# Performance work log

Measured on AMD Instinct MI355X. Metric: run time of the kernel, lower is better.

## Reference

```python
import jax, jax.numpy as jnp
import numpy as np

N = 32768          # total nodes
E = 262144         # edges (before self-loops)
F_IN = 128
H1, H2 = 512, 1024
G = 1024           # graphs (32 nodes each)
NUM_CLASSES = 20
EPS_BN = 1e-5
EPS_LN = 1e-5


def gcn_conv(x, src, dst, W, b, n):
    # PyG GCNConv: add self-loops, symmetric deg^-1/2 normalization,
    # aggregate at target (dst), bias added after aggregation.
    loops = jnp.arange(n)
    s = jnp.concatenate([src, loops])
    d = jnp.concatenate([dst, loops])
    xw = x @ W                                   # [n, out]
    deg = jax.ops.segment_sum(jnp.ones_like(d, dtype=xw.dtype), d, num_segments=n)
    dis = jnp.where(deg > 0, deg ** -0.5, 0.0)
    norm = dis[s] * dis[d]                       # [E+n]
    out = jax.ops.segment_sum(xw[s] * norm[:, None], d, num_segments=n)
    return out + b


def batch_norm(x, w, b):
    # training-mode BatchNorm1d over the node dimension (biased variance)
    mu = x.mean(axis=0)
    var = x.var(axis=0)
    return (x - mu) * jax.lax.rsqrt(var + EPS_BN) * w + b


def graph_layer_norm(x, w, b):
    # PyG LayerNorm(mode='graph') with batch=None: scalar mean/std over ALL
    # elements, eps added to std (not var), per-channel affine.
    mu = x.mean()
    std = jnp.sqrt(((x - mu) ** 2).mean())
    return (x - mu) / (std + EPS_LN) * w + b


def setup_inputs() -> dict:
    key = jax.random.key(0)
    ks = jax.random.split(key, 12)
    x = jax.random.normal(ks[0], (N, F_IN), dtype=jnp.float32)
    edge_index = jax.random.randint(ks[1], (2, E), 0, N, dtype=jnp.int64)
    batch = (jnp.arange(N, dtype=jnp.int64) // (N // G))  # 32 nodes per graph

    def glorot(k, shape):
        lim = np.sqrt(6.0 / (shape[0] + shape[1]))
        return jax.random.uniform(k, shape, jnp.float32, -lim, lim)

    return {
        "x": x,
        "edge_index": edge_index,
        "batch": batch,
        "conv1_w": glorot(ks[2], (F_IN, H1)),
        "conv1_b": jnp.zeros((H1,), jnp.float32),
        "bn1_w": jnp.ones((H1,), jnp.float32),
        "bn1_b": jnp.zeros((H1,), jnp.float32),
        "conv2_w": glorot(ks[3], (H1, H2)),
        "conv2_b": jnp.zeros((H2,), jnp.float32),
        "bn2_w": jnp.ones((H2,), jnp.float32),
        "bn2_b": jnp.zeros((H2,), jnp.float32),
        "ln1_w": jnp.ones((H2,), jnp.float32),
        "ln1_b": jnp.zeros((H2,), jnp.float32),
        "lin1_w": glorot(ks[4], (H2, H1)),
        "lin1_b": jnp.zeros((H1,), jnp.float32),
        "ln2_w": jnp.ones((H1,), jnp.float32),
        "ln2_b": jnp.zeros((H1,), jnp.float32),
        "lin2_w": glorot(ks[5], (H1, NUM_CLASSES)),
        "lin2_b": jnp.zeros((NUM_CLASSES,), jnp.float32),
    }


def reference(x, edge_index, batch, conv1_w, conv1_b, bn1_w, bn1_b,
              conv2_w, conv2_b, bn2_w, bn2_b, ln1_w, ln1_b,
              lin1_w, lin1_b, ln2_w, ln2_b, lin2_w, lin2_b):
    src, dst = edge_index[0], edge_index[1]
    h = jax.nn.relu(batch_norm(gcn_conv(x, src, dst, conv1_w, conv1_b, N), bn1_w, bn1_b))
    # dropout: eval mode -> identity
    h = jax.nn.relu(batch_norm(gcn_conv(h, src, dst, conv2_w, conv2_b, N), bn2_w, bn2_b))
    h = graph_layer_norm(h, ln1_w, ln1_b)
    pooled = jax.ops.segment_max(h, batch, num_segments=G)   # [G, H2]
    z = jax.nn.relu(pooled @ lin1_w + lin1_b)
    z = graph_layer_norm(z, ln2_w, ln2_b)
    logits = z @ lin2_w + lin2_b
    return jax.nn.log_softmax(logits, axis=1)
```

## Files before the change

kernel.cpp:

```cpp
#include <hip/hip_runtime.h>
#include <hip/hip_bf16.h>
#include <hip/hip_fp16.h>

#define NNODES 32768
#define NEDGES 262144
#define FIN    128
#define HID1   512
#define HID2   1024
#define NGRAPH 1024
#define NCLS   20
#define BCAP   64

typedef __attribute__((ext_vector_type(8))) short bf16x8;
typedef __attribute__((ext_vector_type(4))) float f32x4;
typedef __attribute__((ext_vector_type(2))) float f32x2;

__device__ inline float bf2f(unsigned short u) {
    union { unsigned int i; float f; } v; v.i = ((unsigned int)u) << 16; return v.f;
}
__device__ inline unsigned short f2bf(float f) {
    union { unsigned int i; float f; } v; v.f = f;
    unsigned int r = v.i + 0x7FFF + ((v.i >> 16) & 1);
    return (unsigned short)(r >> 16);
}

__device__ inline unsigned char f2e5(float f) {
    unsigned short h = __half_as_ushort(__float2half(f));
    unsigned short r = h + 0x7F + ((h >> 8) & 1);
    return (unsigned char)(r >> 8);
}
__device__ inline float e52f(unsigned char b) {
    return __half2float(__ushort_as_half((unsigned short)(b << 8)));
}

__device__ inline unsigned char f2e4(float f) {
    union { float f; unsigned int i; } v; v.f = f * 0x1p-120f;
    unsigned int b = v.i;
    unsigned int r = b + 0x7FFFF + ((b >> 20) & 1);
    return (unsigned char)(((r >> 20) & 0x7F) | ((b >> 24) & 0x80));
}
__device__ inline float e42f(unsigned char u) {
    union { unsigned int i; float f; } v;
    v.i = ((u & 0x80u) << 24) | ((u & 0x7Fu) << 20);
    return v.f * 0x1p+120f;
}

__device__ inline void e4x8_to_f32(uint2 u, float* v) {
#if __has_builtin(__builtin_amdgcn_cvt_pk_f32_fp8)
    f32x2 p0 = __builtin_amdgcn_cvt_pk_f32_fp8((int)u.x, false);
    f32x2 p1 = __builtin_amdgcn_cvt_pk_f32_fp8((int)u.x, true);
    f32x2 p2 = __builtin_amdgcn_cvt_pk_f32_fp8((int)u.y, false);
    f32x2 p3 = __builtin_amdgcn_cvt_pk_f32_fp8((int)u.y, true);
    v[0] = p0.x; v[1] = p0.y; v[2] = p1.x; v[3] = p1.y;
    v[4] = p2.x; v[5] = p2.y; v[6] = p3.x; v[7] = p3.y;
#else
    const unsigned char* up = (const unsigned char*)&u;
#pragma unroll
    for (int q = 0; q < 8; ++q) v[q] = e42f(up[q]);
#endif
}

typedef unsigned int u32g __attribute__((address_space(1)));
typedef unsigned int u32l __attribute__((address_space(3)));
__device__ inline void load16_lds(const void* g, void* l) {
    __builtin_amdgcn_global_load_lds((const u32g*)g, (u32l*)l, 16, 0, 0);
}

__device__ inline void wtrans_body(const float* __restrict__ W, unsigned short* __restrict__ Wt,
                                   int K, int N, int bx, int by, unsigned short (*tile)[72]) {
    int kb = by * 64, nb = bx * 64;
    {
        int k = threadIdx.x >> 2;
        int n0 = (threadIdx.x & 3) * 16;
#pragma unroll
        for (int q = 0; q < 4; ++q) {
            float4 v = *(const float4*)(W + (size_t)(kb + k) * N + nb + n0 + q * 4);
            tile[k][n0 + q * 4 + 0] = f2bf(v.x);
            tile[k][n0 + q * 4 + 1] = f2bf(v.y);
            tile[k][n0 + q * 4 + 2] = f2bf(v.z);
            tile[k][n0 + q * 4 + 3] = f2bf(v.w);
        }
    }
    __syncthreads();
    {
        int n = threadIdx.x >> 2;
        int k0 = (threadIdx.x & 3) * 16;
#pragma unroll
        for (int q = 0; q < 4; ++q) {
            ushort4 u;
            u.x = tile[k0 + q * 4 + 0][n];
            u.y = tile[k0 + q * 4 + 1][n];
            u.z = tile[k0 + q * 4 + 2][n];
            u.w = tile[k0 + q * 4 + 3][n];
            *(ushort4*)(Wt + (size_t)(nb + n) * K + kb + k0 + q * 4) = u;
        }
    }
}

__global__ __launch_bounds__(256) void prep(const float* __restrict__ x, unsigned short* __restrict__ xb,
                                            const float* __restrict__ W1, unsigned short* __restrict__ w1t,
                                            const float* __restrict__ W2, unsigned short* __restrict__ w2t,
                                            const float* __restrict__ W3, unsigned short* __restrict__ w3t,
                                            float* __restrict__ sF, int* __restrict__ cnt) {
    __shared__ unsigned short tile[64][72];
    int b = blockIdx.x;
    if (b < 168) {
        int t = b * 256 + threadIdx.x;
        if (t < 10240) sF[t] = 0.f;
        if (t < NNODES) cnt[t] = 0;
    } else if (b < 2216) {
        int i = (b - 168) * 256 + threadIdx.x;
        float4 a = ((const float4*)x)[i * 2];
        float4 c = ((const float4*)x)[i * 2 + 1];
        ushort4 u0, u1;
        u0.x = f2bf(a.x); u0.y = f2bf(a.y); u0.z = f2bf(a.z); u0.w = f2bf(a.w);
        u1.x = f2bf(c.x); u1.y = f2bf(c.y); u1.z = f2bf(c.z); u1.w = f2bf(c.w);
        ((ushort4*)xb)[i * 2] = u0;
        ((ushort4*)xb)[i * 2 + 1] = u1;
    } else if (b < 2232) {
        int q = b - 2216;
        wtrans_body(W1, w1t, FIN, HID1, q & 7, q >> 3, tile);
    } else if (b < 2360) {
        int q = b - 2232;
        wtrans_body(W2, w2t, HID1, HID2, q & 15, q >> 4, tile);
    } else {
        int q = b - 2360;
        wtrans_body(W3, w3t, HID2, HID1, q & 7, q >> 3, tile);
    }
}

__global__ __launch_bounds__(256) void bucket_fill(const int* __restrict__ src,
                                                   const int* __restrict__ dst,
                                                   int* __restrict__ cnt,
                                                   int* __restrict__ bucket) {
    int e = blockIdx.x * 256 + threadIdx.x;
    if (e >= NEDGES) return;
    int s = src[e], d = dst[e];
    int pos = atomicAdd(&cnt[d], 1);
    if (pos < BCAP) bucket[((size_t)d << 6) + pos] = s;
}

template<int F, int BNF, int XF8>
__global__ __launch_bounds__(256) void gcn_gather(const void* __restrict__ Xv,
                                                  const int* __restrict__ cnt,
                                                  const int* __restrict__ bucket,
                                                  const float* __restrict__ gsum,
                                                  const float* __restrict__ gsq,
                                                  const float* __restrict__ bw,
                                                  const float* __restrict__ bb,
                                                  float invN,
                                                  unsigned short* __restrict__ out) {
    constexpr int CPL = F / 64;
    int wave = threadIdx.x >> 6, lane = threadIdx.x & 63;
    int node = blockIdx.x * 4 + wave;
    int c0 = lane * CPL;
    float acc[CPL];
#pragma unroll
    for (int q = 0; q < CPL; ++q) acc[q] = 0.f;
    float sc[CPL], sh[CPL];
    if (BNF) {
#pragma unroll
        for (int q = 0; q < CPL; ++q) {
            int ch = c0 + q;
            float mu = gsum[ch] * invN;
            float var = gsq[ch] * invN - mu * mu;
            float s = rsqrtf(var + 1e-5f) * bw[ch];
            sc[q] = s;
            sh[q] = bb[ch] - mu * s;
        }
    }

    const unsigned short* Xc16 = (const unsigned short*)Xv + c0;
    const unsigned char*  Xc8  = (const unsigned char*)Xv + c0;

    auto accum = [&](int s, float w) {
        if (XF8) {
            uint2 u = *(const uint2*)(Xc8 + (size_t)s * F);
            float vv[8];
            e4x8_to_f32(u, vv);
#pragma unroll
            for (int q = 0; q < 8; ++q) {
                float v = vv[q];
                if (BNF) v = fmaxf(v * sc[q] + sh[q], 0.f);
                acc[q] += w * v;
            }
        } else if (CPL == 8) {
            int4 u = *(const int4*)(Xc16 + (size_t)s * F);
            const unsigned short* up = (const unsigned short*)&u;
#pragma unroll
            for (int q = 0; q < 8; ++q) {
                float v = bf2f(up[q]);
                if (BNF) v = fmaxf(v * sc[q] + sh[q], 0.f);
                acc[q] += w * v;
            }
        } else {
            ushort2 u = *(const ushort2*)(Xc16 + (size_t)s * F);
            float v0 = bf2f(u.x), v1 = bf2f(u.y);
            if (BNF) {
                v0 = fmaxf(v0 * sc[0] + sh[0], 0.f);
                v1 = fmaxf(v1 * sc[1] + sh[1], 0.f);
            }
            acc[0] += w * v0; acc[1] += w * v1;
        }
    };

    int deg = cnt[node];
    float di = rsqrtf((float)(deg + 1));
    accum(node, 1.0f / (float)(deg + 1));

    const int* bk = bucket + ((size_t)node << 6);
    int e = 0;
    for (; e + 8 <= deg; e += 8) {
        int4 s0 = *(const int4*)(bk + e);
        int4 s1 = *(const int4*)(bk + e + 4);
        int ss[8] = { s0.x, s0.y, s0.z, s0.w, s1.x, s1.y, s1.z, s1.w };
        float wv[8];
#pragma unroll
        for (int j = 0; j < 8; ++j) wv[j] = di * rsqrtf((float)(cnt[ss[j]] + 1));
#pragma unroll
        for (int j = 0; j < 8; ++j) accum(ss[j], wv[j]);
    }
    for (; e + 4 <= deg; e += 4) {
        int4 s0 = *(const int4*)(bk + e);
        int ss[4] = { s0.x, s0.y, s0.z, s0.w };
        float wv[4];
#pragma unroll
        for (int j = 0; j < 4; ++j) wv[j] = di * rsqrtf((float)(cnt[ss[j]] + 1));
#pragma unroll
        for (int j = 0; j < 4; ++j) accum(ss[j], wv[j]);
    }
    for (; e < deg; ++e) {
        int s = bk[e];
        accum(s, di * rsqrtf((float)(cnt[s] + 1)));
    }

    unsigned short* o = out + (size_t)node * F + c0;
    if (CPL == 2) {
        ushort2 u; u.x = f2bf(acc[0]); u.y = f2bf(acc[1]);
        *(ushort2*)o = u;
    } else {
        ushort4 u0, u1;
        u0.x = f2bf(acc[0]); u0.y = f2bf(acc[1]); u0.z = f2bf(acc[2]); u0.w = f2bf(acc[3]);
        u1.x = f2bf(acc[4]); u1.y = f2bf(acc[5]); u1.z = f2bf(acc[6]); u1.w = f2bf(acc[7]);
        *(ushort4*)o = u0;
        *(ushort4*)(o + 4) = u1;
    }
}

template<int BM, int EPI, int CBF16, int STATS, int POOL, int GSTATS, int CF8>
__global__ __launch_bounds__((BM == 128 ? 256 : 512), 2) void gemm_mfma(
        const unsigned short* __restrict__ A,
        const unsigned short* __restrict__ Bt,
        const float* __restrict__ bias,
        void* __restrict__ Cv,
        float* __restrict__ gsum,
        float* __restrict__ gsq,
        float* __restrict__ gmax,
        float* __restrict__ gmin,
        double* __restrict__ gacc,
        int M, int N, int K) {
    constexpr int BN = 128, BK = 64;
    constexpr int T = (BM == 128) ? 256 : 512;
    constexpr int SMEM_SH = (BM == 128) ? (128 * 136) : ((BM + BN) * BK);
    constexpr int AR = (BM * BK * 2) / (T * 16);
    constexpr int BR = (BN * BK * 2) / (T * 16);
    constexpr int RPR = T / 8;
    __shared__ unsigned short smem[SMEM_SH];
    unsigned short* As = smem;
    unsigned short* Bs = smem + BM * BK;

    const int tid = threadIdx.x;
    const int lane = tid & 63;
    const int wave = tid >> 6;
    const int wr = wave >> 1, wc = wave & 1;

    const int nwg = gridDim.x * gridDim.y;
    const int wg = blockIdx.y * gridDim.x + blockIdx.x;
    const int cpx = nwg >> 3;
    const int swz = (wg & 7) * cpx + (wg >> 3);
    const int m0 = (swz / gridDim.x) * BM, n0 = (swz % gridDim.x) * BN;

    const int sub = ((tid & 7) * 16) ^ (((tid >> 3) & 7) << 4);
    const int rbase = tid >> 3;
    const char* Ab = (const char*)A + sub;
    const char* Bb = (const char*)Bt + sub;

    f32x4 acc[4][4] = {};

    for (int k0 = 0; k0 < K; k0 += BK) {
        __syncthreads();
#pragma unroll
        for (int i = 0; i < AR; ++i) {
            int r = i * RPR + rbase;
            load16_lds(Ab + ((size_t)(m0 + r) * K + k0) * 2, (char*)As + i * (T * 16) + tid * 16);
        }
#pragma unroll
        for (int i = 0; i < BR; ++i) {
            int r = i * RPR + rbase;
            load16_lds(Bb + ((size_t)(n0 + r) * K + k0) * 2, (char*)Bs + i * (T * 16) + tid * 16);
        }
        __syncthreads();
#pragma unroll
        for (int ks = 0; ks < 2; ++ks) {
            bf16x8 af[4], bfr[4];
#pragma unroll
            for (int m = 0; m < 4; ++m) {
                int row = wr * 64 + m * 16 + (lane & 15);
                int s = (ks * 64 + ((lane >> 4) * 16)) ^ ((row & 7) << 4);
                af[m] = *(const bf16x8*)((const char*)As + row * 128 + s);
            }
#pragma unroll
            for (int n = 0; n < 4; ++n) {
                int row = wc * 64 + n * 16 + (lane & 15);
                int s = (ks * 64 + ((lane >> 4) * 16)) ^ ((row & 7) << 4);
                bfr[n] = *(const bf16x8*)((const char*)Bs + row * 128 + s);
            }
#pragma unroll
            for (int m = 0; m < 4; ++m)
#pragma unroll
                for (int n = 0; n < 4; ++n)
                    acc[m][n] = __builtin_amdgcn_mfma_f32_16x16x32_bf16(af[m], bfr[n], acc[m][n], 0, 0, 0);
        }
    }

    if (CBF16) {
        __syncthreads();
        unsigned char* ctile = (unsigned char*)smem;
        float cs[4], cq[4];
        float pmx[2][4], pmn[2][4];
#pragma unroll
        for (int n = 0; n < 4; ++n) {
            cs[n] = 0.f; cq[n] = 0.f;
            if (POOL) {
                pmx[0][n] = -1e30f; pmx[1][n] = -1e30f;
                pmn[0][n] = 1e30f;  pmn[1][n] = 1e30f;
            }
        }
#pragma unroll
        for (int n = 0; n < 4; ++n) {
            int col = wc * 64 + n * 16 + (lane & 15);
            float bsv = bias[n0 + col];
#pragma unroll
            for (int m = 0; m < 4; ++m) {
                int rbase2 = wr * 64 + m * 16 + ((lane >> 4) << 2);
#pragma unroll
                for (int j = 0; j < 4; ++j) {
                    float v = acc[m][n][j] + bsv;
                    if (STATS) { cs[n] += v; cq[n] += v * v; }
                    if (POOL) {
                        pmx[m >> 1][n] = fmaxf(pmx[m >> 1][n], v);
                        pmn[m >> 1][n] = fminf(pmn[m >> 1][n], v);
                    }
                    if (EPI == 1) v = fmaxf(v, 0.f);
                    if (CF8 == 1)      ctile[(rbase2 + j) * 144 + col] = f2e5(v);
                    else if (CF8 == 2) ctile[(rbase2 + j) * 144 + col] = f2e4(v);
                    else if (BM == 128) smem[(rbase2 + j) * 136 + col] = f2bf(v);
                }
            }
        }
        if (STATS) {
#pragma unroll
            for (int n = 0; n < 4; ++n) {
                cs[n] += __shfl_xor(cs[n], 16); cs[n] += __shfl_xor(cs[n], 32);
                cq[n] += __shfl_xor(cq[n], 16); cq[n] += __shfl_xor(cq[n], 32);
            }
            if (lane < 16) {
#pragma unroll
                for (int n = 0; n < 4; ++n) {
                    int col = n0 + wc * 64 + n * 16 + lane;
                    atomicAdd(&gsum[col], cs[n]);
                    atomicAdd(&gsq[col],  cq[n]);
                }
            }
        }
        if (POOL) {
#pragma unroll
            for (int gi = 0; gi < 2; ++gi)
#pragma unroll
                for (int n = 0; n < 4; ++n) {
                    pmx[gi][n] = fmaxf(pmx[gi][n], __shfl_xor(pmx[gi][n], 16));
                    pmx[gi][n] = fmaxf(pmx[gi][n], __shfl_xor(pmx[gi][n], 32));
                    pmn[gi][n] = fminf(pmn[gi][n], __shfl_xor(pmn[gi][n], 16));
                    pmn[gi][n] = fminf(pmn[gi][n], __shfl_xor(pmn[gi][n], 32));
                }
            if (lane < 16) {
                int gb = (m0 >> 5) + wr * 2;
#pragma unroll
                for (int gi = 0; gi < 2; ++gi)
#pragma unroll
                    for (int n = 0; n < 4; ++n) {
                        int col = n0 + wc * 64 + n * 16 + lane;
                        gmax[(size_t)(gb + gi) * HID2 + col] = pmx[gi][n];
                        gmin[(size_t)(gb + gi) * HID2 + col] = pmn[gi][n];
                    }
            }
        }
        __syncthreads();
        if (CF8) {
#pragma unroll
            for (int it = 0; it < (BM * 8) / T; ++it) {
                int l = it * T + tid;
                int r = l >> 3, ch = l & 7;
                int4 v = *(const int4*)(ctile + r * 144 + ch * 16);
                *(int4*)((unsigned char*)Cv + (size_t)(m0 + r) * N + n0 + ch * 16) = v;
            }
        } else if (BM == 128) {
#pragma unroll
            for (int it = 0; it < 8; ++it) {
                int r = it * 16 + (tid >> 4);
                int ch = tid & 15;
                int4 v = *(const int4*)&smem[r * 136 + ch * 8];
                *(int4*)((unsigned short*)Cv + (size_t)(m0 + r) * N + n0 + ch * 8) = v;
            }
        }
    } else {
        float ls = 0.f, lq = 0.f;
#pragma unroll
        for (int m = 0; m < 4; ++m) {
            int row = m0 + wr * 64 + m * 16 + ((lane >> 4) << 2);
#pragma unroll
            for (int n = 0; n < 4; ++n) {
                int col = n0 + wc * 64 + n * 16 + (lane & 15);
                float bsv = bias[col];
#pragma unroll
                for (int j = 0; j < 4; ++j) {
                    float v = acc[m][n][j] + bsv;
                    if (EPI == 1) v = fmaxf(v, 0.f);
                    if (GSTATS) { ls += v; lq += v * v; }
                    ((float*)Cv)[(size_t)(row + j) * N + col] = v;
                }
            }
        }
        if (GSTATS) {
            for (int o = 32; o > 0; o >>= 1) {
                ls += __shfl_down(ls, o);
                lq += __shfl_down(lq, o);
            }
            if (lane == 0) {
                atomicAdd(gacc,     (double)ls);
                atomicAdd(gacc + 1, (double)lq);
            }
        }
    }
}

__global__ __launch_bounds__(256) void lnstats_h2(const unsigned char* __restrict__ H,
                                                  const float* __restrict__ gsum,
                                                  const float* __restrict__ gsq,
                                                  const float* __restrict__ bw,
                                                  const float* __restrict__ bb,
                                                  float invN,
                                                  double* __restrict__ lnacc) {
    int half = threadIdx.x >> 7;
    int c0 = (threadIdx.x & 127) * 8;
    float sc[8], sh[8];
#pragma unroll
    for (int q = 0; q < 8; ++q) {
        int ch = c0 + q;
        float mu = gsum[ch] * invN;
        float var = gsq[ch] * invN - mu * mu;
        float s = rsqrtf(var + 1e-5f) * bw[ch];
        sc[q] = s;
        sh[q] = bb[ch] - mu * s;
    }
    float lsum = 0.f, lsq = 0.f;
    for (int r = blockIdx.x * 2 + half; r < NNODES; r += gridDim.x * 2) {
        uint2 u = *(const uint2*)(H + (size_t)r * HID2 + c0);
        const unsigned char* up = (const unsigned char*)&u;
#pragma unroll
        for (int q = 0; q < 8; ++q) {
            float v = fmaxf(e52f(up[q]) * sc[q] + sh[q], 0.f);
            lsum += v; lsq += v * v;
        }
    }
    for (int o = 32; o > 0; o >>= 1) {
        lsum += __shfl_down(lsum, o);
        lsq  += __shfl_down(lsq, o);
    }
    __shared__ float w1[4], w2[4];
    int wid = threadIdx.x >> 6, lane = threadIdx.x & 63;
    if (lane == 0) { w1[wid] = lsum; w2[wid] = lsq; }
    __syncthreads();
    if (threadIdx.x == 0) {
        atomicAdd(lnacc,     (double)(w1[0] + w1[1] + w1[2] + w1[3]));
        atomicAdd(lnacc + 1, (double)(w2[0] + w2[1] + w2[2] + w2[3]));
    }
}

__global__ __launch_bounds__(256) void pool_fin(const float* __restrict__ gmax,
                                                const float* __restrict__ gmin,
                                                const float* __restrict__ bsum,
                                                const float* __restrict__ bsq,
                                                const float* __restrict__ bw,
                                                const float* __restrict__ bb,
                                                const double* __restrict__ lnacc,
                                                const float* __restrict__ lw,
                                                const float* __restrict__ lb,
                                                float invN, double invCnt,
                                                unsigned short* __restrict__ P) {
    int i = blockIdx.x * 256 + threadIdx.x;
    int c0 = (i * 4) & (HID2 - 1);
    double dmu = lnacc[0] * invCnt;
    double dvar = lnacc[1] * invCnt - dmu * dmu;
    if (dvar < 0.0) dvar = 0.0;
    float smu = (float)dmu;
    float sinv = 1.0f / (sqrtf((float)dvar) + 1e-5f);
    float4 mx = ((const float4*)gmax)[i];
    float4 mn = ((const float4*)gmin)[i];
    float r[4];
    const float* mxp = (const float*)&mx;
    const float* mnp = (const float*)&mn;
#pragma unroll
    for (int q = 0; q < 4; ++q) {
        int ch = c0 + q;
        float bmu = bsum[ch] * invN;
        float bvar = bsq[ch] * invN - bmu * bmu;
        float s = rsqrtf(bvar + 1e-5f) * bw[ch];
        float t = bb[ch] - bmu * s;
        float A = sinv * lw[ch];
        float C = lb[ch] - smu * A;
        float vs = ((s >= 0.f) == (A >= 0.f)) ? mxp[q] : mnp[q];
        r[q] = A * fmaxf(s * vs + t, 0.f) + C;
    }
    ushort4 o;
    o.x = f2bf(r[0]); o.y = f2bf(r[1]); o.z = f2bf(r[2]); o.w = f2bf(r[3]);
    ((ushort4*)P)[i] = o;
}

__global__ __launch_bounds__(256) void gemm4_lsm(const float* __restrict__ Z,
                                                 const double* __restrict__ acc2,
                                                 const float* __restrict__ lw,
                                                 const float* __restrict__ lb,
                                                 const float* __restrict__ W,
                                                 const float* __restrict__ bias,
                                                 double invCnt,
                                                 float* __restrict__ out) {
    __shared__ float zs[HID1];
    __shared__ float part[8][NCLS];
    __shared__ float logits[NCLS];
    __shared__ float smaxs, slse;
    int m = blockIdx.x;
    double dmu = acc2[0] * invCnt;
    double dvar = acc2[1] * invCnt - dmu * dmu;
    if (dvar < 0.0) dvar = 0.0;
    float smu = (float)dmu;
    float sinv = 1.0f / (sqrtf((float)dvar) + 1e-5f);
    for (int k = threadIdx.x; k < HID1; k += 256) {
        float A = sinv * lw[k];
        zs[k] = Z[(size_t)m * HID1 + k] * A + (lb[k] - smu * A);
    }
    __syncthreads();
    int t = threadIdx.x;
    if (t < 160) {
        int c = t >> 3, s = t & 7;
        float a = 0.f;
        int k0 = s * 64;
#pragma unroll 8
        for (int k = k0; k < k0 + 64; ++k)
            a += zs[k] * W[k * NCLS + c];
        part[s][c] = a;
    }
    __syncthreads();
    if (t < NCLS) {
        float a = bias[t];
#pragma unroll
        for (int s = 0; s < 8; ++s) a += part[s][t];
        logits[t] = a;
    }
    __syncthreads();
    if (t == 0) {
        float mx = -1e30f;
        for (int j = 0; j < NCLS; ++j) mx = fmaxf(mx, logits[j]);
        float s = 0.f;
        for (int j = 0; j < NCLS; ++j) s += expf(logits[j] - mx);
        smaxs = mx; slse = logf(s);
    }
    __syncthreads();
    if (t < NCLS)
        out[(size_t)m * NCLS + t] = logits[t] - smaxs - slse;
}

extern "C" void kernel_launch(void* const* d_in, const int* in_sizes, int n_in,
                              void* d_out, int out_size, void* d_ws, size_t ws_size,
                              hipStream_t stream) {
    const float* x       = (const float*)d_in[0];
    const int*   ei      = (const int*)d_in[1];
    const int*   src     = ei;
    const int*   dst     = ei + NEDGES;
    const float* conv1_w = (const float*)d_in[3];
    const float* conv1_b = (const float*)d_in[4];
    const float* bn1_w   = (const float*)d_in[5];
    const float* bn1_b   = (const float*)d_in[6];
    const float* conv2_w = (const float*)d_in[7];
    const float* conv2_b = (const float*)d_in[8];
    const float* bn2_w   = (const float*)d_in[9];
    const float* bn2_b   = (const float*)d_in[10];
    const float* ln1_w   = (const float*)d_in[11];
    const float* ln1_b   = (const float*)d_in[12];
    const float* lin1_w  = (const float*)d_in[13];
    const float* lin1_b  = (const float*)d_in[14];
    const float* ln2_w   = (const float*)d_in[15];
    const float* ln2_b   = (const float*)d_in[16];
    const float* lin2_w  = (const float*)d_in[17];
    const float* lin2_b  = (const float*)d_in[18];
    float* out = (float*)d_out;

    char* ws = (char*)d_ws;
    const size_t KB = 1024, MB = 1048576;
    float*          sF      = (float*)(ws + 128 * KB);
    unsigned short* w1t     = (unsigned short*)(ws + 256 * KB);
    unsigned short* w2t     = (unsigned short*)(ws + 512 * KB);
    unsigned short* w3t     = (unsigned short*)(ws + 1536 * KB);
    int*            cnt     = (int*)(ws + 2560 * KB);
    unsigned short* pool    = (unsigned short*)(ws + 5 * MB);
    float*          z       = (float*)(ws + 7 * MB);
    unsigned short* agg1    = (unsigned short*)(ws + 16 * MB);
    unsigned char*  h1      = (unsigned char*)(ws + 24 * MB);
    unsigned char*  h2      = (unsigned char*)(ws + 16 * MB);
    int*            bucket  = (int*)(ws + 48 * MB);
    float*          gmax    = (float*)(ws + 80 * MB);
    float*          gmin    = (float*)(ws + 84 * MB);
    unsigned short* agg2    = (unsigned short*)(ws + 88 * MB);
    unsigned short* xb      = (unsigned short*)(ws + 120 * MB);

    float* bn1_sum = sF + 0,      *bn1_sq    = sF + 512;
    float* bn2_sum = sF + 2048,   *bn2_sq    = sF + 3072;
    double* lnacc = (double*)(sF + 9216);

    const float invN = 1.0f / (float)NNODES;

    prep<<<2488, 256, 0, stream>>>(x, xb, conv1_w, w1t, conv2_w, w2t, lin1_w, w3t, sF, cnt);

    bucket_fill<<<(NEDGES + 255) / 256, 256, 0, stream>>>(src, dst, cnt, bucket);

    gcn_gather<FIN, 0, 0><<<NNODES / 4, 256, 0, stream>>>(xb, cnt, bucket,
                                                          nullptr, nullptr, nullptr, nullptr, 0.f, agg1);
    gemm_mfma<256, 0, 1, 1, 0, 0, 2><<<dim3(HID1 / 128, NNODES / 256), 512, 0, stream>>>(
        agg1, w1t, conv1_b, h1, bn1_sum, bn1_sq, nullptr, nullptr, nullptr, NNODES, HID1, FIN);

    gcn_gather<HID1, 1, 1><<<NNODES / 4, 256, 0, stream>>>(h1, cnt, bucket,
                                                           bn1_sum, bn1_sq, bn1_w, bn1_b, invN, agg2);
    gemm_mfma<256, 0, 1, 1, 1, 0, 1><<<dim3(HID2 / 128, NNODES / 256), 512, 0, stream>>>(
        agg2, w2t, conv2_b, h2, bn2_sum, bn2_sq, gmax, gmin, nullptr, NNODES, HID2, HID1);

    lnstats_h2<<<1024, 256, 0, stream>>>(h2, bn2_sum, bn2_sq, bn2_w, bn2_b, invN, lnacc);

    pool_fin<<<NGRAPH * HID2 / 4 / 256, 256, 0, stream>>>(
        gmax, gmin, bn2_sum, bn2_sq, bn2_w, bn2_b, lnacc, ln1_w, ln1_b,
        invN, 1.0 / ((double)NNODES * HID2), pool);

    gemm_mfma<128, 1, 0, 0, 0, 1, 0><<<dim3(HID1 / 128, NGRAPH / 128), 256, 0, stream>>>(
        pool, w3t, lin1_b, z, nullptr, nullptr, nullptr, nullptr, lnacc + 2, NGRAPH, HID1, HID2);

    gemm4_lsm<<<NGRAPH, 256, 0, stream>>>(z, lnacc + 2, ln2_w, ln2_b, lin2_w, lin2_b,
                                          1.0 / ((double)NGRAPH * HID1), out);
}
```

Measured before the change: 215.6 us.

## Fuse tail stages into one cooperative kernel with grid syncs

Replaces the four tail launches (layer-norm stats, pooling finalize, lin1 GEMM, lin2 with log-softmax) with a single cooperative kernel that separates the phases using grid.sync. This removes three kernel launch gaps and their inter-kernel drains. In exchange the kernel needs all 1024 blocks co-resident, only 32 blocks do work during the GEMM phase, and grid syncs have their own cost. The old launch sequence is kept as a fallback if the cooperative launch fails.

Result: slower. 527.5 us (+144.6%).

```diff
diff --git a/kernel.cpp b/kernel.cpp
--- a/kernel.cpp
+++ b/kernel.cpp
@@ -1,6 +1,9 @@
 #include <hip/hip_runtime.h>
 #include <hip/hip_bf16.h>
 #include <hip/hip_fp16.h>
+#include <hip/hip_cooperative_groups.h>
+
+namespace cg = cooperative_groups;
 
 #define NNODES 32768
 #define NEDGES 262144
@@ -580,6 +583,217 @@
         out[(size_t)m * NCLS + t] = logits[t] - smaxs - slse;
 }
 
+struct TailArgs {
+    const unsigned char* h2;
+    const float* bn2_sum; const float* bn2_sq;
+    const float* bn2_w;   const float* bn2_b;
+    float invN;
+    double* lnacc;
+    const float* gmax; const float* gmin;
+    const float* ln1_w; const float* ln1_b;
+    double invCnt1;
+    unsigned short* pool;
+    const unsigned short* w3t;
+    const float* lin1_b;
+    float* z;
+    const float* ln2_w; const float* ln2_b;
+    const float* lin2_w; const float* lin2_b;
+    double invCnt2;
+    float* out;
+};
+
+__global__ __launch_bounds__(256, 4) void tail_coop(TailArgs a) {
+    cg::grid_group grid = cg::this_grid();
+    __shared__ unsigned short smem[128 * 136];
+    const int bid = blockIdx.x;
+    const int tid = threadIdx.x;
+    const int lane = tid & 63, wid = tid >> 6;
+
+    {
+        int half = tid >> 7;
+        int c0 = (tid & 127) * 8;
+        float sc[8], sh[8];
+#pragma unroll
+        for (int q = 0; q < 8; ++q) {
+            int ch = c0 + q;
+            float mu = a.bn2_sum[ch] * a.invN;
+            float var = a.bn2_sq[ch] * a.invN - mu * mu;
+            float s = rsqrtf(var + 1e-5f) * a.bn2_w[ch];
+            sc[q] = s;
+            sh[q] = a.bn2_b[ch] - mu * s;
+        }
+        float lsum = 0.f, lsq = 0.f;
+        for (int r = bid * 2 + half; r < NNODES; r += 2048) {
+            uint2 u = *(const uint2*)(a.h2 + (size_t)r * HID2 + c0);
+            const unsigned char* up = (const unsigned char*)&u;
+#pragma unroll
+            for (int q = 0; q < 8; ++q) {
+                float v = fmaxf(e52f(up[q]) * sc[q] + sh[q], 0.f);
+                lsum += v; lsq += v * v;
+            }
+        }
+        for (int o = 32; o > 0; o >>= 1) {
+            lsum += __shfl_down(lsum, o);
+            lsq  += __shfl_down(lsq, o);
+        }
+        float* w1 = (float*)smem;
+        float* w2 = w1 + 4;
+        if (lane == 0) { w1[wid] = lsum; w2[wid] = lsq; }
+        __syncthreads();
+        if (tid == 0) {
+            atomicAdd(a.lnacc,     (double)(w1[0] + w1[1] + w1[2] + w1[3]));
+            atomicAdd(a.lnacc + 1, (double)(w2[0] + w2[1] + w2[2] + w2[3]));
+        }
+    }
+    grid.sync();
+
+    {
+        int i = bid * 256 + tid;
+        int c0 = (i * 4) & (HID2 - 1);
+        double dmu = a.lnacc[0] * a.invCnt1;
+        double dvar = a.lnacc[1] * a.invCnt1 - dmu * dmu;
+        if (dvar < 0.0) dvar = 0.0;
+        float smu = (float)dmu;
+        float sinv = 1.0f / (sqrtf((float)dvar) + 1e-5f);
+        float4 mx = ((const float4*)a.gmax)[i];
+        float4 mn = ((const float4*)a.gmin)[i];
+        float r[4];
+        const float* mxp = (const float*)&mx;
+        const float* mnp = (const float*)&mn;
+#pragma unroll
+        for (int q = 0; q < 4; ++q) {
+            int ch = c0 + q;
+            float bmu = a.bn2_sum[ch] * a.invN;
+            float bvar = a.bn2_sq[ch] * a.invN - bmu * bmu;
+            float s = rsqrtf(bvar + 1e-5f) * a.bn2_w[ch];
+            float t = a.bn2_b[ch] - bmu * s;
+            float A = sinv * a.ln1_w[ch];
+            float C = a.ln1_b[ch] - smu * A;
+            float vs = ((s >= 0.f) == (A >= 0.f)) ? mxp[q] : mnp[q];
+            r[q] = A * fmaxf(s * vs + t, 0.f) + C;
+        }
+        ushort4 o;
+        o.x = f2bf(r[0]); o.y = f2bf(r[1]); o.z = f2bf(r[2]); o.w = f2bf(r[3]);
+        ((ushort4*)a.pool)[i] = o;
+    }
+    grid.sync();
+
+    if (bid < 32) {
+        const int wr = wid >> 1, wc = wid & 1;
+        const int swz = (bid & 7) * 4 + (bid >> 3);
+        const int m0 = (swz >> 2) * 128, n0 = (swz & 3) * 128;
+        const int sub = ((tid & 7) * 16) ^ (((tid >> 3) & 7) << 4);
+        const int rbase = tid >> 3;
+        const char* Ab = (const char*)a.pool + sub;
+        const char* Bb = (const char*)a.w3t + sub;
+        unsigned short* As = smem;
+        unsigned short* Bs = smem + 128 * 64;
+        f32x4 acc[4][4] = {};
+        for (int k0 = 0; k0 < HID2; k0 += 64) {
+            __syncthreads();
+#pragma unroll
+            for (int i = 0; i < 4; ++i) {
+                int r = i * 32 + rbase;
+                load16_lds(Ab + ((size_t)(m0 + r) * HID2 + k0) * 2, (char*)As + i * 4096 + tid * 16);
+                load16_lds(Bb + ((size_t)(n0 + r) * HID2 + k0) * 2, (char*)Bs + i * 4096 + tid * 16);
+            }
+            __syncthreads();
+#pragma unroll
+            for (int ks = 0; ks < 2; ++ks) {
+                bf16x8 af[4], bfr[4];
+#pragma unroll
+                for (int m = 0; m < 4; ++m) {
+                    int row = wr * 64 + m * 16 + (lane & 15);
+                    int s = (ks * 64 + ((lane >> 4) * 16)) ^ ((row & 7) << 4);
+                    af[m] = *(const bf16x8*)((const char*)As + row * 128 + s);
+                }
+#pragma unroll
+                for (int n = 0; n < 4; ++n) {
+                    int row = wc * 64 + n * 16 + (lane & 15);
+                    int s = (ks * 64 + ((lane >> 4) * 16)) ^ ((row & 7) << 4);
+                    bfr[n] = *(const bf16x8*)((const char*)Bs + row * 128 + s);
+                }
+#pragma unroll
+                for (int m = 0; m < 4; ++m)
+#pragma unroll
+                    for (int n = 0; n < 4; ++n)
+                        acc[m][n] = __builtin_amdgcn_mfma_f32_16x16x32_bf16(af[m], bfr[n], acc[m][n], 0, 0, 0);
+            }
+        }
+        float ls = 0.f, lq = 0.f;
+#pragma unroll
+        for (int m = 0; m < 4; ++m) {
+            int row = m0 + wr * 64 + m * 16 + ((lane >> 4) << 2);
+#pragma unroll
+            for (int n = 0; n < 4; ++n) {
+                int col = n0 + wc * 64 + n * 16 + (lane & 15);
+                float bsv = a.lin1_b[col];
+#pragma unroll
+                for (int j = 0; j < 4; ++j) {
+                    float v = fmaxf(acc[m][n][j] + bsv, 0.f);
+                    ls += v; lq += v * v;
+                    a.z[(size_t)(row + j) * HID1 + col] = v;
+                }
+            }
+        }
+        for (int o = 32; o > 0; o >>= 1) {
+            ls += __shfl_down(ls, o);
+            lq += __shfl_down(lq, o);
+        }
+        if (lane == 0) {
+            atomicAdd(a.lnacc + 2, (double)ls);
+            atomicAdd(a.lnacc + 3, (double)lq);
+        }
+    }
+    grid.sync();
+
+    {
+        float* zs = (float*)smem;
+        float* part = zs + HID1;
+        float* logits = part + 8 * NCLS;
+        float* red = logits + NCLS;
+        int m = bid;
+        double dmu = a.lnacc[2] * a.invCnt2;
+        double dvar = a.lnacc[3] * a.invCnt2 - dmu * dmu;
+        if (dvar < 0.0) dvar = 0.0;
+        float smu = (float)dmu;
+        float sinv = 1.0f / (sqrtf((float)dvar) + 1e-5f);
+        __syncthreads();
+        for (int k = tid; k < HID1; k += 256) {
+            float A = sinv * a.ln2_w[k];
+            zs[k] = a.z[(size_t)m * HID1 + k] * A + (a.ln2_b[k] - smu * A);
+        }
+        __syncthreads();
+        if (tid < 160) {
+            int c = tid >> 3, s = tid & 7;
+            float av = 0.f;
+            int k0 = s * 64;
+#pragma unroll 8
+            for (int k = k0; k < k0 + 64; ++k)
+                av += zs[k] * a.lin2_w[k * NCLS + c];
+            part[s * NCLS + c] = av;
+        }
+        __syncthreads();
+        if (tid < NCLS) {
+            float av = a.lin2_b[tid];
+#pragma unroll
+            for (int s = 0; s < 8; ++s) av += part[s * NCLS + tid];
+            logits[tid] = av;
+        }
+        __syncthreads();
+        if (tid == 0) {
+            float mx = -1e30f;
+            for (int j = 0; j < NCLS; ++j) mx = fmaxf(mx, logits[j]);
+            float s = 0.f;
+            for (int j = 0; j < NCLS; ++j) s += expf(logits[j] - mx);
+            red[0] = mx; red[1] = logf(s);
+        }
+        __syncthreads();
+        if (tid < NCLS)
+            a.out[(size_t)m * NCLS + tid] = logits[tid] - red[0] - red[1];
+    }
+}
+
 extern "C" void kernel_launch(void* const* d_in, const int* in_sizes, int n_in,
                               void* d_out, int out_size, void* d_ws, size_t ws_size,
                               hipStream_t stream) {
@@ -628,6 +842,8 @@
     double* lnacc = (double*)(sF + 9216);
 
     const float invN = 1.0f / (float)NNODES;
+    const double invCnt1 = 1.0 / ((double)NNODES * HID2);
+    const double invCnt2 = 1.0 / ((double)NGRAPH * HID1);
 
     prep<<<2488, 256, 0, stream>>>(x, xb, conv1_w, w1t, conv2_w, w2t, lin1_w, w3t, sF, cnt);
 
@@ -643,15 +859,24 @@
     gemm_mfma<256, 0, 1, 1, 1, 0, 1><<<dim3(HID2 / 128, NNODES / 256), 512, 0, stream>>>(
         agg2, w2t, conv2_b, h2, bn2_sum, bn2_sq, gmax, gmin, nullptr, NNODES, HID2, HID1);
 
-    lnstats_h2<<<1024, 256, 0, stream>>>(h2, bn2_sum, bn2_sq, bn2_w, bn2_b, invN, lnacc);
-
-    pool_fin<<<NGRAPH * HID2 / 4 / 256, 256, 0, stream>>>(
-        gmax, gmin, bn2_sum, bn2_sq, bn2_w, bn2_b, lnacc, ln1_w, ln1_b,
-        invN, 1.0 / ((double)NNODES * HID2), pool);
-
-    gemm_mfma<128, 1, 0, 0, 0, 1, 0><<<dim3(HID1 / 128, NGRAPH / 128), 256, 0, stream>>>(
-        pool, w3t, lin1_b, z, nullptr, nullptr, nullptr, nullptr, lnacc + 2, NGRAPH, HID1, HID2);
-
-    gemm4_lsm<<<NGRAPH, 256, 0, stream>>>(z, lnacc + 2, ln2_w, ln2_b, lin2_w, lin2_b,
-                                          1.0 / ((double)NGRAPH * HID1), out);
-}
+    TailArgs ta;
+    ta.h2 = h2; ta.bn2_sum = bn2_sum; ta.bn2_sq = bn2_sq; ta.bn2_w = bn2_w; ta.bn2_b = bn2_b;
+    ta.invN = invN; ta.lnacc = lnacc; ta.gmax = gmax; ta.gmin = gmin;
+    ta.ln1_w = ln1_w; ta.ln1_b = ln1_b; ta.invCnt1 = invCnt1;
+    ta.pool = pool; ta.w3t = w3t; ta.lin1_b = lin1_b; ta.z = z;
+    ta.ln2_w = ln2_w; ta.ln2_b = ln2_b; ta.lin2_w = lin2_w; ta.lin2_b = lin2_b;
+    ta.invCnt2 = invCnt2; ta.out = out;
+    void* kargs[] = { &ta };
+    hipError_t cerr = hipLaunchCooperativeKernel((const void*)tail_coop, dim3(1024), dim3(256),
+                                                 kargs, 0, stream);
+    if (cerr != hipSuccess) {
+        lnstats_h2<<<1024, 256, 0, stream>>>(h2, bn2_sum, bn2_sq, bn2_w, bn2_b, invN, lnacc);
+        pool_fin<<<NGRAPH * HID2 / 4 / 256, 256, 0, stream>>>(
+            gmax, gmin, bn2_sum, bn2_sq, bn2_w, bn2_b, lnacc, ln1_w, ln1_b,
+            invN, invCnt1, pool);
+        gemm_mfma<128, 1, 0, 0, 0, 1, 0><<<dim3(HID1 / 128, NGRAPH / 128), 256, 0, stream>>>(
+            pool, w3t, lin1_b, z, nullptr, nullptr, nullptr, nullptr, lnacc + 2, NGRAPH, HID1, HID2);
+        gemm4_lsm<<<NGRAPH, 256, 0, stream>>>(z, lnacc + 2, ln2_w, ln2_b, lin2_w, lin2_b,
+                                              invCnt2, out);
+    }
+}
```
